# Kernel optimization log

Hardware: AMD Instinct MI355X
Metric: run time of the kernel (lower is better)

## Reference

```python
import jax, jax.numpy as jnp
import numpy as np

INPUT_DIM = 512
HIDDEN_DIM = 1024
OUTPUT_DIM = 512
SEQ_LEN = 16384


def setup_inputs() -> dict:
    key = jax.random.key(0)
    ks = jax.random.split(key, 8)
    s = 1.0 / np.sqrt(HIDDEN_DIM)
    X = jax.random.normal(ks[0], (SEQ_LEN, INPUT_DIM), dtype=jnp.float32)
    # PyTorch GRU params: weight_ih [3H, D], weight_hh [3H, H], biases [3H]; gate order r, z, n
    W_ih = jax.random.uniform(ks[1], (3 * HIDDEN_DIM, INPUT_DIM), minval=-s, maxval=s, dtype=jnp.float32)
    W_hh = jax.random.uniform(ks[2], (3 * HIDDEN_DIM, HIDDEN_DIM), minval=-s, maxval=s, dtype=jnp.float32)
    b_ih = jax.random.uniform(ks[3], (3 * HIDDEN_DIM,), minval=-s, maxval=s, dtype=jnp.float32)
    b_hh = jax.random.uniform(ks[4], (3 * HIDDEN_DIM,), minval=-s, maxval=s, dtype=jnp.float32)
    W_fc = jax.random.uniform(ks[5], (OUTPUT_DIM, HIDDEN_DIM), minval=-s, maxval=s, dtype=jnp.float32)
    b_fc = jax.random.uniform(ks[6], (OUTPUT_DIM,), minval=-s, maxval=s, dtype=jnp.float32)
    return {"X": X, "W_ih": W_ih, "W_hh": W_hh, "b_ih": b_ih, "b_hh": b_hh, "W_fc": W_fc, "b_fc": b_fc}


def _gru_seq(X, W_ih, W_hh, b_ih, b_hh):
    H = W_hh.shape[1]
    # Precompute input projections for all timesteps in one GEMM: [T, 3H]
    gx = X @ W_ih.T + b_ih

    def step(h, gx_t):
        gxr, gxz, gxn = gx_t[:H], gx_t[H:2 * H], gx_t[2 * H:]
        gh = h @ W_hh.T + b_hh
        ghr, ghz, ghn = gh[:H], gh[H:2 * H], gh[2 * H:]
        r = jax.nn.sigmoid(gxr + ghr)
        z = jax.nn.sigmoid(gxz + ghz)
        n = jnp.tanh(gxn + r * ghn)
        h_new = (1.0 - z) * n + z * h
        return h_new, h_new

    h0 = jnp.zeros((H,), dtype=X.dtype)
    _, hs = jax.lax.scan(step, h0, gx)  # hs: [T, H]
    return hs


def reference(X, W_ih, W_hh, b_ih, b_hh, W_fc, b_fc):
    hs = _gru_seq(X, W_ih, W_hh, b_ih, b_hh)  # [T, H]
    return hs @ W_fc.T + b_fc  # [T, output_dim]
```

## Files before the change

kernel.cpp:

```cpp
#include <hip/hip_runtime.h>
#include <hip/hip_bf16.h>

#define H      1024
#define IN_DIM 512
#define OD     512
#define T_LEN  16384
#define NWG    256
#define NREP   8

typedef unsigned long long u64;
typedef unsigned int u32;

__device__ __forceinline__ u32 pack_bf(float lo, float hi) {
    u32 a = __float_as_uint(lo); a = (a + 0x7fffu + ((a >> 16) & 1u)) >> 16;
    u32 b = __float_as_uint(hi); b = (b + 0x7fffu + ((b >> 16) & 1u)) & 0xffff0000u;
    return a | b;
}
__device__ __forceinline__ float bf_lo(u32 pk) { return __uint_as_float(pk << 16); }
__device__ __forceinline__ float bf_hi(u32 pk) { return __uint_as_float(pk & 0xffff0000u); }

__global__ __launch_bounds__(256, 1)
void gru_rec_kernel(const float* __restrict__ X,
                    const float* __restrict__ Wih,
                    const float* __restrict__ Whh,
                    const float* __restrict__ bih,
                    const float* __restrict__ bhh,
                    float* __restrict__ hs,
                    u64* __restrict__ pairs)
{
    __shared__ float hsh[H];

    const int tid  = threadIdx.x;
    const int wave = tid >> 6;
    const int lane = tid & 63;
    const int wg   = blockIdx.x;
    const int u    = wg * 4 + wave;

    u32 whh_r[3][8];
    u32 wih_r[3][4];
    #pragma unroll
    for (int g = 0; g < 3; ++g) {
        const float* wr = Whh + (size_t)(g * H + u) * H;
        #pragma unroll
        for (int c = 0; c < 8; ++c)
            whh_r[g][c] = pack_bf(wr[2 * lane + 128 * c], wr[2 * lane + 1 + 128 * c]);
        const float* wx = Wih + (size_t)(g * H + u) * IN_DIM;
        #pragma unroll
        for (int c = 0; c < 4; ++c)
            wih_r[g][c] = pack_bf(wx[2 * lane + 128 * c], wx[2 * lane + 1 + 128 * c]);
    }
    const float bxr = bih[u], bxz = bih[H + u], bxn = bih[2 * H + u];
    const float bhr = bhh[u], bhz = bhh[H + u], bhn = bhh[2 * H + u];

    float xv[8], xw[8];
    #pragma unroll
    for (int c = 0; c < 4; ++c) {
        float2 v = *(const float2*)(X + 2 * lane + 128 * c);
        xv[2 * c] = v.x; xv[2 * c + 1] = v.y;
    }

    const int rdu = (tid + wg * 4) & 255;
    u64* const prep = pairs + (size_t)(wg & (NREP - 1)) * 2 * H;

    #pragma unroll 1
    for (int t = 0; t < T_LEN; ++t) {
        float xr = 0.f, xz = 0.f, xn = 0.f;
        #pragma unroll
        for (int c = 0; c < 4; ++c) {
            const float x0 = xv[2 * c], x1 = xv[2 * c + 1];
            xr += bf_lo(wih_r[0][c]) * x0 + bf_hi(wih_r[0][c]) * x1;
            xz += bf_lo(wih_r[1][c]) * x0 + bf_hi(wih_r[1][c]) * x1;
            xn += bf_lo(wih_r[2][c]) * x0 + bf_hi(wih_r[2][c]) * x1;
        }
        float xns = xn;
        #pragma unroll
        for (int s = 32; s; s >>= 1) xns += __shfl_xor(xns, s, 64);

        {
            const int tn = (t + 1 < T_LEN) ? (t + 1) : t;
            const float* xp = X + (size_t)tn * IN_DIM;
            #pragma unroll
            for (int c = 0; c < 4; ++c) {
                float2 v = *(const float2*)(xp + 2 * lane + 128 * c);
                xw[2 * c] = v.x; xw[2 * c + 1] = v.y;
            }
        }

        u64* pp = prep + (size_t)(t & 1) * H + rdu * 4;
        const u32 want = (u32)t;
        u64 p0, p1, p2, p3;
        for (;;) {
            p0 = __hip_atomic_load(pp + 0, __ATOMIC_RELAXED, __HIP_MEMORY_SCOPE_AGENT);
            p1 = __hip_atomic_load(pp + 1, __ATOMIC_RELAXED, __HIP_MEMORY_SCOPE_AGENT);
            p2 = __hip_atomic_load(pp + 2, __ATOMIC_RELAXED, __HIP_MEMORY_SCOPE_AGENT);
            p3 = __hip_atomic_load(pp + 3, __ATOMIC_RELAXED, __HIP_MEMORY_SCOPE_AGENT);
            if ((u32)(p0 >> 32) == want && (u32)(p1 >> 32) == want &&
                (u32)(p2 >> 32) == want && (u32)(p3 >> 32) == want) break;
        }
        {
            float4 hv4 = make_float4(__uint_as_float((u32)p0), __uint_as_float((u32)p1),
                                     __uint_as_float((u32)p2), __uint_as_float((u32)p3));
            *(float4*)&hsh[rdu * 4] = hv4;
        }
        __syncthreads();

        if (t && wg == (t & (NWG - 1))) {
            float4 hv4 = *(const float4*)&hsh[tid * 4];
            *(float4*)(hs + (size_t)(t - 1) * H + tid * 4) = hv4;
        }

        float ar = xr, az = xz, anh = 0.f;
        #pragma unroll
        for (int c = 0; c < 8; ++c) {
            float2 h2 = *(const float2*)&hsh[2 * lane + 128 * c];
            ar  += bf_lo(whh_r[0][c]) * h2.x + bf_hi(whh_r[0][c]) * h2.y;
            az  += bf_lo(whh_r[1][c]) * h2.x + bf_hi(whh_r[1][c]) * h2.y;
            anh += bf_lo(whh_r[2][c]) * h2.x + bf_hi(whh_r[2][c]) * h2.y;
        }

        #pragma unroll
        for (int s = 32; s; s >>= 1) {
            ar  += __shfl_xor(ar,  s, 64);
            az  += __shfl_xor(az,  s, 64);
            anh += __shfl_xor(anh, s, 64);
        }

        if (lane == 0) {
            const float hprev = hsh[u];
            const float r = 1.f / (1.f + __expf(-(ar + bxr + bhr)));
            const float z = 1.f / (1.f + __expf(-(az + bxz + bhz)));
            const float e2 = __expf(2.f * (xns + bxn + r * (anh + bhn)));
            const float n = 1.f - 2.f / (e2 + 1.f);
            const float hnew = (1.f - z) * n + z * hprev;
            const u64 pk = ((u64)(u32)(t + 1) << 32) | (u64)__float_as_uint(hnew);
            const size_t slot = (size_t)((t + 1) & 1) * H + u;
            #pragma unroll
            for (int rp = 0; rp < NREP; ++rp)
                __hip_atomic_store(pairs + (size_t)rp * 2 * H + slot, pk,
                                   __ATOMIC_RELAXED, __HIP_MEMORY_SCOPE_AGENT);
            if (t == T_LEN - 1)
                hs[(size_t)t * H + u] = hnew;
        }
        __syncthreads();

        #pragma unroll
        for (int i = 0; i < 8; ++i) xv[i] = xw[i];
    }
}

#define BM 64
#define BN 64
#define BK 16
__global__ __launch_bounds__(256)
void fc_kernel(const float* __restrict__ A, const float* __restrict__ B,
               const float* __restrict__ bias, float* __restrict__ C)
{
    __shared__ float As[BK][BM + 4];
    __shared__ float Bs[BK][BN + 4];
    const int tid = threadIdx.x;
    const int m0 = blockIdx.y * BM, n0 = blockIdx.x * BN;
    const int tx = tid & 15, ty = tid >> 4;
    float acc[4][4] = {};
    const int r = tid >> 2, c = (tid & 3) << 2;
    for (int k0 = 0; k0 < H; k0 += BK) {
        float4 va = *(const float4*)(A + (size_t)(m0 + r) * H + (k0 + c));
        As[c + 0][r] = va.x; As[c + 1][r] = va.y; As[c + 2][r] = va.z; As[c + 3][r] = va.w;
        float4 vb = *(const float4*)(B + (size_t)(n0 + r) * H + (k0 + c));
        Bs[c + 0][r] = vb.x; Bs[c + 1][r] = vb.y; Bs[c + 2][r] = vb.z; Bs[c + 3][r] = vb.w;
        __syncthreads();
        #pragma unroll
        for (int kk = 0; kk < BK; ++kk) {
            float4 a4 = *(const float4*)&As[kk][ty * 4];
            float4 b4 = *(const float4*)&Bs[kk][tx * 4];
            const float av[4] = {a4.x, a4.y, a4.z, a4.w};
            const float bv[4] = {b4.x, b4.y, b4.z, b4.w};
            #pragma unroll
            for (int i = 0; i < 4; ++i)
                #pragma unroll
                for (int j = 0; j < 4; ++j)
                    acc[i][j] += av[i] * bv[j];
        }
        __syncthreads();
    }
    #pragma unroll
    for (int i = 0; i < 4; ++i) {
        const int m = m0 + ty * 4 + i;
        #pragma unroll
        for (int j = 0; j < 4; ++j) {
            const int n = n0 + tx * 4 + j;
            C[(size_t)m * OD + n] = acc[i][j] + bias[n];
        }
    }
}

extern "C" void kernel_launch(void* const* d_in, const int* in_sizes, int n_in,
                              void* d_out, int out_size, void* d_ws, size_t ws_size,
                              hipStream_t stream) {
    const float* X   = (const float*)d_in[0];
    const float* Wih = (const float*)d_in[1];
    const float* Whh = (const float*)d_in[2];
    const float* bih = (const float*)d_in[3];
    const float* bhh = (const float*)d_in[4];
    const float* Wfc = (const float*)d_in[5];
    const float* bfc = (const float*)d_in[6];
    float* out = (float*)d_out;

    float* hs    = (float*)d_ws;
    u64*   pairs = (u64*)((char*)d_ws + (size_t)T_LEN * H * 4);

    hipMemsetAsync(pairs, 0, (size_t)NREP * 2 * H * sizeof(u64), stream);

    void* args[] = { (void*)&X, (void*)&Wih, (void*)&Whh, (void*)&bih,
                     (void*)&bhh, (void*)&hs, (void*)&pairs };
    hipError_t e = hipLaunchCooperativeKernel((const void*)gru_rec_kernel,
                                              dim3(NWG), dim3(256), args, 0, stream);
    if (e != hipSuccess) {
        gru_rec_kernel<<<dim3(NWG), dim3(256), 0, stream>>>(X, Wih, Whh, bih, bhh, hs, pairs);
    }

    dim3 fgrid(OD / BN, T_LEN / BM);
    fc_kernel<<<fgrid, dim3(256), 0, stream>>>(hs, Wfc, bfc, out);
}
```

Before: 31.38 ms.

## Replace tagged 64-bit exchange and LDS barriers with per-wave LSB-lap-tagged polling

Each wave now polls its own 16 contiguous hidden values straight from globally replicated buffers with sc0 sc1 vector loads, and uses the low mantissa bit as a parity lap flag instead of a 32-bit step tag. This removes the shared-memory staging and both __syncthreads per step, halves exchange traffic, and raises the replica count from 8 to 32 with padded rows to spread polling contention. Weights are re-laid out so each lane owns a contiguous 16-element slice. The cost is one mantissa bit of hidden-state precision, and a parity scheme that relies on no wave being more than one lap ahead.

```diff
diff --git a/kernel.cpp b/kernel.cpp
--- a/kernel.cpp
+++ b/kernel.cpp
@@ -6,7 +6,9 @@
 #define OD     512
 #define T_LEN  16384
 #define NWG    256
-#define NREP   8
+#define NREP   32
+#define RS     (H + 64)
+#define PSTRIDE (NREP * RS)
 
 typedef unsigned long long u64;
 typedef unsigned int u32;
@@ -18,6 +20,22 @@
 }
 __device__ __forceinline__ float bf_lo(u32 pk) { return __uint_as_float(pk << 16); }
 __device__ __forceinline__ float bf_hi(u32 pk) { return __uint_as_float(pk & 0xffff0000u); }
+
+__device__ __forceinline__ void llc_load64(const u32* p, uint4& a, uint4& b, uint4& c, uint4& d) {
+    u64 addr = (u64)p;
+    asm volatile(
+        "global_load_dwordx4 %0, %4, off sc0 sc1\n\t"
+        "global_load_dwordx4 %1, %4, off offset:16 sc0 sc1\n\t"
+        "global_load_dwordx4 %2, %4, off offset:32 sc0 sc1\n\t"
+        "global_load_dwordx4 %3, %4, off offset:48 sc0 sc1\n\t"
+        "s_waitcnt vmcnt(0)"
+        : "=&v"(a), "=&v"(b), "=&v"(c), "=&v"(d)
+        : "v"(addr)
+        : "memory");
+}
+__device__ __forceinline__ u32 lapdiff(uint4 c, u32 lap) {
+    return ((c.x ^ lap) | (c.y ^ lap) | (c.z ^ lap) | (c.w ^ lap)) & 1u;
+}
 
 __global__ __launch_bounds__(256, 1)
 void gru_rec_kernel(const float* __restrict__ X,
@@ -26,24 +44,23 @@
                     const float* __restrict__ bih,
                     const float* __restrict__ bhh,
                     float* __restrict__ hs,
-                    u64* __restrict__ pairs)
+                    u32* __restrict__ vals)
 {
-    __shared__ float hsh[H];
-
     const int tid  = threadIdx.x;
     const int wave = tid >> 6;
     const int lane = tid & 63;
     const int wg   = blockIdx.x;
-    const int u    = wg * 4 + wave;
+    const int gw   = wg * 4 + wave;
+    const int u    = gw;
 
     u32 whh_r[3][8];
     u32 wih_r[3][4];
     #pragma unroll
     for (int g = 0; g < 3; ++g) {
-        const float* wr = Whh + (size_t)(g * H + u) * H;
+        const float* wr = Whh + (size_t)(g * H + u) * H + 16 * lane;
         #pragma unroll
         for (int c = 0; c < 8; ++c)
-            whh_r[g][c] = pack_bf(wr[2 * lane + 128 * c], wr[2 * lane + 1 + 128 * c]);
+            whh_r[g][c] = pack_bf(wr[2 * c], wr[2 * c + 1]);
         const float* wx = Wih + (size_t)(g * H + u) * IN_DIM;
         #pragma unroll
         for (int c = 0; c < 4; ++c)
@@ -59,8 +76,8 @@
         xv[2 * c] = v.x; xv[2 * c + 1] = v.y;
     }
 
-    const int rdu = (tid + wg * 4) & 255;
-    u64* const prep = pairs + (size_t)(wg & (NREP - 1)) * 2 * H;
+    const u32* const mybase = vals + (size_t)(wg & (NREP - 1)) * RS + 16 * lane;
+    float hmine = 0.f;
 
     #pragma unroll 1
     for (int t = 0; t < T_LEN; ++t) {
@@ -86,38 +103,37 @@
             }
         }
 
-        u64* pp = prep + (size_t)(t & 1) * H + rdu * 4;
-        const u32 want = (u32)t;
-        u64 p0, p1, p2, p3;
+        const u32 lapexp = (u32)((t >> 1) & 1);
+        const u32* pbase = mybase + (size_t)(t & 1) * PSTRIDE;
+        uint4 c0, c1, c2, c3;
         for (;;) {
-            p0 = __hip_atomic_load(pp + 0, __ATOMIC_RELAXED, __HIP_MEMORY_SCOPE_AGENT);
-            p1 = __hip_atomic_load(pp + 1, __ATOMIC_RELAXED, __HIP_MEMORY_SCOPE_AGENT);
-            p2 = __hip_atomic_load(pp + 2, __ATOMIC_RELAXED, __HIP_MEMORY_SCOPE_AGENT);
-            p3 = __hip_atomic_load(pp + 3, __ATOMIC_RELAXED, __HIP_MEMORY_SCOPE_AGENT);
-            if ((u32)(p0 >> 32) == want && (u32)(p1 >> 32) == want &&
-                (u32)(p2 >> 32) == want && (u32)(p3 >> 32) == want) break;
-        }
-        {
-            float4 hv4 = make_float4(__uint_as_float((u32)p0), __uint_as_float((u32)p1),
-                                     __uint_as_float((u32)p2), __uint_as_float((u32)p3));
-            *(float4*)&hsh[rdu * 4] = hv4;
-        }
-        __syncthreads();
-
-        if (t && wg == (t & (NWG - 1))) {
-            float4 hv4 = *(const float4*)&hsh[tid * 4];
-            *(float4*)(hs + (size_t)(t - 1) * H + tid * 4) = hv4;
-        }
+            llc_load64(pbase, c0, c1, c2, c3);
+            if (!(lapdiff(c0, lapexp) | lapdiff(c1, lapexp) |
+                  lapdiff(c2, lapexp) | lapdiff(c3, lapexp))) break;
+        }
+
+        if (t && gw == ((t - 1) & (H - 1))) {
+            float* dst = hs + (size_t)(t - 1) * H + 16 * lane;
+            *(uint4*)(dst + 0)  = c0;
+            *(uint4*)(dst + 4)  = c1;
+            *(uint4*)(dst + 8)  = c2;
+            *(uint4*)(dst + 12) = c3;
+        }
+
+        float hv[16];
+        hv[0]=__uint_as_float(c0.x); hv[1]=__uint_as_float(c0.y); hv[2]=__uint_as_float(c0.z); hv[3]=__uint_as_float(c0.w);
+        hv[4]=__uint_as_float(c1.x); hv[5]=__uint_as_float(c1.y); hv[6]=__uint_as_float(c1.z); hv[7]=__uint_as_float(c1.w);
+        hv[8]=__uint_as_float(c2.x); hv[9]=__uint_as_float(c2.y); hv[10]=__uint_as_float(c2.z); hv[11]=__uint_as_float(c2.w);
+        hv[12]=__uint_as_float(c3.x); hv[13]=__uint_as_float(c3.y); hv[14]=__uint_as_float(c3.z); hv[15]=__uint_as_float(c3.w);
 
         float ar = xr, az = xz, anh = 0.f;
         #pragma unroll
         for (int c = 0; c < 8; ++c) {
-            float2 h2 = *(const float2*)&hsh[2 * lane + 128 * c];
-            ar  += bf_lo(whh_r[0][c]) * h2.x + bf_hi(whh_r[0][c]) * h2.y;
-            az  += bf_lo(whh_r[1][c]) * h2.x + bf_hi(whh_r[1][c]) * h2.y;
-            anh += bf_lo(whh_r[2][c]) * h2.x + bf_hi(whh_r[2][c]) * h2.y;
-        }
-
+            const float h0 = hv[2 * c], h1 = hv[2 * c + 1];
+            ar  += bf_lo(whh_r[0][c]) * h0 + bf_hi(whh_r[0][c]) * h1;
+            az  += bf_lo(whh_r[1][c]) * h0 + bf_hi(whh_r[1][c]) * h1;
+            anh += bf_lo(whh_r[2][c]) * h0 + bf_hi(whh_r[2][c]) * h1;
+        }
         #pragma unroll
         for (int s = 32; s; s >>= 1) {
             ar  += __shfl_xor(ar,  s, 64);
@@ -125,23 +141,19 @@
             anh += __shfl_xor(anh, s, 64);
         }
 
-        if (lane == 0) {
-            const float hprev = hsh[u];
-            const float r = 1.f / (1.f + __expf(-(ar + bxr + bhr)));
-            const float z = 1.f / (1.f + __expf(-(az + bxz + bhz)));
-            const float e2 = __expf(2.f * (xns + bxn + r * (anh + bhn)));
-            const float n = 1.f - 2.f / (e2 + 1.f);
-            const float hnew = (1.f - z) * n + z * hprev;
-            const u64 pk = ((u64)(u32)(t + 1) << 32) | (u64)__float_as_uint(hnew);
-            const size_t slot = (size_t)((t + 1) & 1) * H + u;
-            #pragma unroll
-            for (int rp = 0; rp < NREP; ++rp)
-                __hip_atomic_store(pairs + (size_t)rp * 2 * H + slot, pk,
-                                   __ATOMIC_RELAXED, __HIP_MEMORY_SCOPE_AGENT);
-            if (t == T_LEN - 1)
-                hs[(size_t)t * H + u] = hnew;
-        }
-        __syncthreads();
+        const float r = 1.f / (1.f + __expf(-(ar + bxr + bhr)));
+        const float z = 1.f / (1.f + __expf(-(az + bxz + bhz)));
+        const float e2 = __expf(2.f * (xns + bxn + r * (anh + bhn)));
+        const float n = 1.f - 2.f / (e2 + 1.f);
+        const float hnew = (1.f - z) * n + z * hmine;
+        const u32 lapw = (u32)(((t + 1) >> 1) & 1);
+        const u32 bits = (__float_as_uint(hnew) & ~1u) | lapw;
+        hmine = __uint_as_float(bits);
+        if (lane < NREP)
+            __hip_atomic_store(vals + (size_t)((t + 1) & 1) * PSTRIDE + (size_t)lane * RS + u,
+                               bits, __ATOMIC_RELAXED, __HIP_MEMORY_SCOPE_AGENT);
+        if (t == T_LEN - 1 && lane == 0)
+            hs[(size_t)t * H + u] = hmine;
 
         #pragma unroll
         for (int i = 0; i < 8; ++i) xv[i] = xw[i];
@@ -205,17 +217,18 @@
     const float* bfc = (const float*)d_in[6];
     float* out = (float*)d_out;
 
-    float* hs    = (float*)d_ws;
-    u64*   pairs = (u64*)((char*)d_ws + (size_t)T_LEN * H * 4);
-
-    hipMemsetAsync(pairs, 0, (size_t)NREP * 2 * H * sizeof(u64), stream);
+    float* hs  = (float*)d_ws;
+    u32*  vals = (u32*)((char*)d_ws + (size_t)T_LEN * H * 4);
+
+    hipMemsetAsync(vals, 0x00, (size_t)PSTRIDE * 4, stream);
+    hipMemsetAsync(vals + PSTRIDE, 0x01, (size_t)PSTRIDE * 4, stream);
 
     void* args[] = { (void*)&X, (void*)&Wih, (void*)&Whh, (void*)&bih,
-                     (void*)&bhh, (void*)&hs, (void*)&pairs };
+                     (void*)&bhh, (void*)&hs, (void*)&vals };
     hipError_t e = hipLaunchCooperativeKernel((const void*)gru_rec_kernel,
                                               dim3(NWG), dim3(256), args, 0, stream);
     if (e != hipSuccess) {
-        gru_rec_kernel<<<dim3(NWG), dim3(256), 0, stream>>>(X, Wih, Whh, bih, bhh, hs, pairs);
+        gru_rec_kernel<<<dim3(NWG), dim3(256), 0, stream>>>(X, Wih, Whh, bih, bhh, hs, vals);
     }
 
     dim3 fgrid(OD / BN, T_LEN / BM);
```

New measurement: 39.76 ms. +26.7%, slower.
